# Performance work log

Hardware: AMD Instinct MI355X
Metric: run time of the kernel (lower is better)

The kernel has to match this reference:

```python
import jax, jax.numpy as jnp
import numpy as np

# Config matching init_kwargs: 63 single-grapheme tokens + optional blank -> C = 64,
# trivial (identity) lexicon, ngram = 0 (no transition model), allow_repeats = True.
# Under this config the GTN composition (target chain o lexicon -> tokens graph ->
# alignments, intersected with linear emission graph, forward_score) is exactly the
# CTC forward algorithm over the extended label sequence z = [blank, y1, blank, ...,
# yL, blank], with the s-2 -> s skip allowed for ALL non-blank states (allow_repeats).

B, T, C, L = 128, 3000, 64, 128
NEG = -1e30  # effective -inf, safe in fp32


def setup_inputs() -> dict:
    key = jax.random.key(0)
    k1, k2 = jax.random.split(key)
    inputs = jax.random.normal(k1, (B, T, C), dtype=jnp.float32)  # raw logits
    # target token ids in [0, C-2]; blank = C-1 is never a target
    targets = jax.random.randint(k2, (B, L), 0, C - 1, dtype=jnp.int32)
    return {"inputs": inputs, "targets": targets}


def reference(inputs, targets):
    Bv, Tv, Cv = inputs.shape
    Lv = targets.shape[1]
    S = 2 * Lv + 1
    blank = Cv - 1
    # transitions is None -> module applies log_softmax to inputs
    logp = jax.nn.log_softmax(inputs, axis=2)  # [B, T, C]
    # extended label sequence: blanks at even positions, targets at odd positions
    z = jnp.full((Bv, S), blank, dtype=jnp.int32).at[:, 1::2].set(targets)  # [B, S]
    # per-frame emission scores for each extended state: [B, T, S] -> [T, B, S]
    em = jnp.take_along_axis(logp, jnp.broadcast_to(z[:, None, :], (Bv, Tv, S)), axis=2)
    em = jnp.transpose(em, (1, 0, 2))
    # skip transition (s-2 -> s) allowed for every non-blank (odd) state because
    # allow_repeats=True (no z[s] != z[s-2] restriction)
    skip_ok = (jnp.arange(S) % 2 == 1)  # [S]

    alpha0 = (jnp.full((Bv, S), NEG, dtype=jnp.float32)
              .at[:, 0].set(em[0, :, 0])
              .at[:, 1].set(em[0, :, 1]))

    def step(alpha, e_t):
        a1 = jnp.pad(alpha[:, :-1], ((0, 0), (1, 0)), constant_values=NEG)
        a2 = jnp.pad(alpha[:, :-2], ((0, 0), (2, 0)), constant_values=NEG)
        a2 = jnp.where(skip_ok[None, :], a2, NEG)
        new = e_t + jax.scipy.special.logsumexp(jnp.stack([alpha, a1, a2], axis=0), axis=0)
        return new, None

    alphaT, _ = jax.lax.scan(step, alpha0, em[1:])  # [B, S]
    # accepting states: last label (S-2) and trailing blank (S-1)
    ll = jax.scipy.special.logsumexp(alphaT[:, S - 2:S], axis=1)  # [B]
    # reduction='none' -> scales = 1; forward returns torch.mean over batch
    return jnp.mean(-ll)
```

## Files before the change

kernel.cpp:

```cpp
#include <hip/hip_runtime.h>
#include <stdint.h>

#define BB 128
#define TT 3000
#define CC 64
#define LL 128
#define NEG (-1e30f)
#define LOG2E 1.4426950408889634f
#define LN2f 0.6931471805599453f
#define F 24
#define NCH 125
#define LSE_BLOCKS 512

typedef float f32x2 __attribute__((ext_vector_type(2)));

__device__ __forceinline__ float fexp2(float x) { return __builtin_amdgcn_exp2f(x); }
__device__ __forceinline__ float flog2(float x) { return __builtin_amdgcn_logf(x); }

__device__ __forceinline__ float lse2(float x, float y) {
    float m = fmaxf(x, y);
    float e = fexp2(-fabsf(x - y));
    return m + flog2(1.0f + e);
}
__device__ __forceinline__ float shr1_neg(float x) {
    int r = __builtin_amdgcn_update_dpp(__float_as_int(NEG), __float_as_int(x),
                                        0x138 , 0xF, 0xF, false);
    return __int_as_float(r);
}
#define SBAR() __builtin_amdgcn_sched_barrier(0)

__global__ __launch_bounds__(512) void fused_kernel(const float* __restrict__ in,
                                                    const int* __restrict__ tgt,
                                                    float* __restrict__ lse,
                                                    float* __restrict__ ll2) {
    __shared__ f32x2 ring[2][F][64];
    __shared__ float ringB[2][F];
    if (blockIdx.x < BB) {
        const int b = blockIdx.x;
        const int wave = threadIdx.x >> 6;
        const int lane = threadIdx.x & 63;
        const float* fb = in + (size_t)b * TT * CC;
        const int t0 = tgt[b * LL + 2 * lane];
        const int t1 = tgt[b * LL + 2 * lane + 1];

#define PRODUCE(cc, nb) {                                                        \
            const int tb_ = (cc) * F;                                            \
            const int p_ = wave - 1;                                             \
            float w1_[4], w3_[4], wb_[4];                                        \
            _Pragma("unroll")                                                    \
            for (int k = 0; k < 4; ++k) {                                        \
                int f_ = p_ + k * 7;                                             \
                if (f_ < F) {                                                    \
                    const float* fr_ = fb + (size_t)(tb_ + f_) * CC;             \
                    w1_[k] = fr_[t0]; w3_[k] = fr_[t1]; wb_[k] = fr_[63];        \
                }                                                                \
            }                                                                    \
            _Pragma("unroll")                                                    \
            for (int k = 0; k < 4; ++k) {                                        \
                int f_ = p_ + k * 7;                                             \
                if (f_ < F) {                                                    \
                    f32x2 v_; v_.x = w1_[k] * LOG2E; v_.y = w3_[k] * LOG2E;      \
                    ring[nb][f_][lane] = v_;                                     \
                    if (lane == 0) ringB[nb][f_] = wb_[k] * LOG2E;               \
                }                                                                \
            }                                                                    \
        }

        if (wave > 0) PRODUCE(0, 0);
        __syncthreads();

        if (wave == 0) {
            __builtin_amdgcn_s_setprio(1);
            const uint32_t ring_base =
                (uint32_t)(uintptr_t)&ring[0][0][0] + (uint32_t)lane * 8u;
            const uint32_t rb_base = (uint32_t)(uintptr_t)&ringB[0][0];

            float a0 = (lane == 0) ? 0.f : NEG;
            float a1 = NEG, a2 = NEG, a3 = NEG, a4 = NEG;

            for (int c = 0; c < NCH; ++c) {
                const uint32_t ra = ring_base + (uint32_t)(c & 1) * (F * 64 * 8);
                const uint32_t rb = rb_base + (uint32_t)(c & 1) * (F * 4);
                f32x2 e0, e1, e2; float b0, b1, b2;
                asm volatile("ds_read_b64 %0, %1 offset:0"   : "=v"(e0) : "v"(ra));
                asm volatile("ds_read_b32 %0, %1 offset:0"   : "=v"(b0) : "v"(rb));
                asm volatile("ds_read_b64 %0, %1 offset:512" : "=v"(e1) : "v"(ra));
                asm volatile("ds_read_b32 %0, %1 offset:4"   : "=v"(b1) : "v"(rb));
                #pragma unroll
                for (int j = 0; j < F; ++j) {
                    if (j + 2 < F) {
                        asm volatile("ds_read_b64 %0, %1 offset:%2"
                                     : "=v"(e2) : "v"(ra), "n"((j + 2) * 512));
                        asm volatile("ds_read_b32 %0, %1 offset:%2"
                                     : "=v"(b2) : "v"(rb), "n"((j + 2) * 4));
                        asm volatile("s_waitcnt lgkmcnt(4)" ::: "memory");
                    } else if (j + 2 == F) {
                        asm volatile("s_waitcnt lgkmcnt(2)" ::: "memory");
                    } else {
                        asm volatile("s_waitcnt lgkmcnt(0)" ::: "memory");
                    }
                    SBAR();
                    float pp = shr1_neg(a3);
                    float t_ = lse2(a0, pp);
                    float n0 = b0 + t_;
                    float n1 = e0.x + lse2(a1, t_);
                    float u_ = lse2(a2, a1);
                    float n2 = b0 + u_;
                    float n3 = e0.y + lse2(a3, u_);
                    float n4 = b0 + lse2(a4, a3);
                    a0 = n0; a1 = n1; a2 = n2; a3 = n3; a4 = n4;
                    e0 = e1; b0 = b1; e1 = e2; b1 = b2;
                }
                __syncthreads();
            }
            if (lane == 63) ll2[b] = lse2(a3, a4);
        } else {
            for (int c = 0; c < NCH; ++c) {
                if (c + 1 < NCH) PRODUCE(c + 1, (c + 1) & 1);
                __syncthreads();
            }
        }
        return;
    }
    int w = (blockIdx.x - BB) * 8 + (threadIdx.x >> 6);
    int lane = threadIdx.x & 63;
    const int stride = LSE_BLOCKS * 8;
    for (int row = w; row < BB * TT; row += stride) {
        float x = in[(size_t)row * CC + lane];
        float m = x;
        #pragma unroll
        for (int d = 32; d >= 1; d >>= 1) m = fmaxf(m, __shfl_xor(m, d, 64));
        float s = fexp2((x - m) * LOG2E);
        #pragma unroll
        for (int d = 32; d >= 1; d >>= 1) s += __shfl_xor(s, d, 64);
        if (lane == 0) lse[row] = m + flog2(s) * LN2f;
    }
}

__global__ __launch_bounds__(256) void bsum_kernel(const float* __restrict__ lse,
                                                   const float* __restrict__ ll2,
                                                   float* __restrict__ lossb) {
    __shared__ float red[256];
    int b = blockIdx.x;
    float s = 0.f;
    for (int i = threadIdx.x; i < TT; i += 256) s += lse[(size_t)b * TT + i];
    red[threadIdx.x] = s;
    __syncthreads();
    #pragma unroll
    for (int w = 128; w >= 1; w >>= 1) {
        if (threadIdx.x < w) red[threadIdx.x] += red[threadIdx.x + w];
        __syncthreads();
    }
    if (threadIdx.x == 0) lossb[b] = red[0] - ll2[b] * LN2f;
}

__global__ __launch_bounds__(64) void final_kernel(const float* __restrict__ lossb,
                                                   float* __restrict__ out) {
    int lane = threadIdx.x;
    float v = lossb[lane] + lossb[lane + 64];
    #pragma unroll
    for (int d = 32; d >= 1; d >>= 1) v += __shfl_xor(v, d, 64);
    if (lane == 0) out[0] = v / (float)BB;
}

extern "C" void kernel_launch(void* const* d_in, const int* in_sizes, int n_in,
                              void* d_out, int out_size, void* d_ws, size_t ws_size,
                              hipStream_t stream) {
    const float* in = (const float*)d_in[0];
    const int* tg = (const int*)d_in[1];
    float* out = (float*)d_out;
    float* lse = (float*)d_ws;
    float* ll2 = lse + (size_t)BB * TT;
    float* lossb = ll2 + BB;

    hipLaunchKernelGGL(fused_kernel, dim3(BB + LSE_BLOCKS), dim3(512), 0, stream,
                       in, tg, lse, ll2);
    hipLaunchKernelGGL(bsum_kernel, dim3(BB), dim3(256), 0, stream, lse, ll2, lossb);
    hipLaunchKernelGGL(final_kernel, dim3(1), dim3(64), 0, stream, lossb, out);
}
```

Before: 292.3 us.

## Split CTC alpha recursion across two waves with skewed pipelined boundary exchange

The serial CTC forward recursion, which previously ran five states per lane in one wave, is split across two waves that each hold two or three states per lane. The first wave covers the first half of the labels and writes its last lane's alpha into a shared boundary buffer each frame. The second wave runs one chunk behind and reads that boundary value. A three-slot emission ring makes room for the skew, and the producers drop to six waves. This shortens the per-frame dependency chain on the critical wave, at the cost of extra LDS traffic, a lag of one chunk, and an extra barrier phase.

New measurement: 241.2 us. 1.21x faster.

```diff
diff --git a/kernel.cpp b/kernel.cpp
--- a/kernel.cpp
+++ b/kernel.cpp
@@ -12,8 +12,6 @@
 #define NCH 125
 #define LSE_BLOCKS 512
 
-typedef float f32x2 __attribute__((ext_vector_type(2)));
-
 __device__ __forceinline__ float fexp2(float x) { return __builtin_amdgcn_exp2f(x); }
 __device__ __forceinline__ float flog2(float x) { return __builtin_amdgcn_logf(x); }
 
@@ -33,92 +31,153 @@
                                                     const int* __restrict__ tgt,
                                                     float* __restrict__ lse,
                                                     float* __restrict__ ll2) {
-    __shared__ f32x2 ring[2][F][64];
-    __shared__ float ringB[2][F];
+    __shared__ float ringT[3][F][128];
+    __shared__ float ringBl[3][F];
+    __shared__ float bndr[3][F];
+    __shared__ float dump[64];
     if (blockIdx.x < BB) {
         const int b = blockIdx.x;
         const int wave = threadIdx.x >> 6;
         const int lane = threadIdx.x & 63;
         const float* fb = in + (size_t)b * TT * CC;
-        const int t0 = tgt[b * LL + 2 * lane];
-        const int t1 = tgt[b * LL + 2 * lane + 1];
-
-#define PRODUCE(cc, nb) {                                                        \
-            const int tb_ = (cc) * F;                                            \
-            const int p_ = wave - 1;                                             \
-            float w1_[4], w3_[4], wb_[4];                                        \
-            _Pragma("unroll")                                                    \
-            for (int k = 0; k < 4; ++k) {                                        \
-                int f_ = p_ + k * 7;                                             \
-                if (f_ < F) {                                                    \
-                    const float* fr_ = fb + (size_t)(tb_ + f_) * CC;             \
-                    w1_[k] = fr_[t0]; w3_[k] = fr_[t1]; wb_[k] = fr_[63];        \
-                }                                                                \
-            }                                                                    \
-            _Pragma("unroll")                                                    \
-            for (int k = 0; k < 4; ++k) {                                        \
-                int f_ = p_ + k * 7;                                             \
-                if (f_ < F) {                                                    \
-                    f32x2 v_; v_.x = w1_[k] * LOG2E; v_.y = w3_[k] * LOG2E;      \
-                    ring[nb][f_][lane] = v_;                                     \
-                    if (lane == 0) ringB[nb][f_] = wb_[k] * LOG2E;               \
-                }                                                                \
-            }                                                                    \
-        }
-
-        if (wave > 0) PRODUCE(0, 0);
-        __syncthreads();
-
-        if (wave == 0) {
-            __builtin_amdgcn_s_setprio(1);
-            const uint32_t ring_base =
-                (uint32_t)(uintptr_t)&ring[0][0][0] + (uint32_t)lane * 8u;
-            const uint32_t rb_base = (uint32_t)(uintptr_t)&ringB[0][0];
-
-            float a0 = (lane == 0) ? 0.f : NEG;
-            float a1 = NEG, a2 = NEG, a3 = NEG, a4 = NEG;
-
-            for (int c = 0; c < NCH; ++c) {
-                const uint32_t ra = ring_base + (uint32_t)(c & 1) * (F * 64 * 8);
-                const uint32_t rb = rb_base + (uint32_t)(c & 1) * (F * 4);
-                f32x2 e0, e1, e2; float b0, b1, b2;
-                asm volatile("ds_read_b64 %0, %1 offset:0"   : "=v"(e0) : "v"(ra));
-                asm volatile("ds_read_b32 %0, %1 offset:0"   : "=v"(b0) : "v"(rb));
-                asm volatile("ds_read_b64 %0, %1 offset:512" : "=v"(e1) : "v"(ra));
-                asm volatile("ds_read_b32 %0, %1 offset:4"   : "=v"(b1) : "v"(rb));
+
+        if (wave >= 2) {
+            const int p = wave - 2;
+            const int t0 = tgt[b * LL + lane];
+            const int t1 = tgt[b * LL + 64 + lane];
+            auto produce = [&](int cc) {
+                const int slot = cc % 3;
+                const float* base = fb + (size_t)cc * F * CC;
+                float v0[4], v1[4], vb[4];
                 #pragma unroll
-                for (int j = 0; j < F; ++j) {
-                    if (j + 2 < F) {
-                        asm volatile("ds_read_b64 %0, %1 offset:%2"
-                                     : "=v"(e2) : "v"(ra), "n"((j + 2) * 512));
-                        asm volatile("ds_read_b32 %0, %1 offset:%2"
-                                     : "=v"(b2) : "v"(rb), "n"((j + 2) * 4));
-                        asm volatile("s_waitcnt lgkmcnt(4)" ::: "memory");
-                    } else if (j + 2 == F) {
-                        asm volatile("s_waitcnt lgkmcnt(2)" ::: "memory");
-                    } else {
-                        asm volatile("s_waitcnt lgkmcnt(0)" ::: "memory");
-                    }
-                    SBAR();
-                    float pp = shr1_neg(a3);
-                    float t_ = lse2(a0, pp);
-                    float n0 = b0 + t_;
-                    float n1 = e0.x + lse2(a1, t_);
-                    float u_ = lse2(a2, a1);
-                    float n2 = b0 + u_;
-                    float n3 = e0.y + lse2(a3, u_);
-                    float n4 = b0 + lse2(a4, a3);
-                    a0 = n0; a1 = n1; a2 = n2; a3 = n3; a4 = n4;
-                    e0 = e1; b0 = b1; e1 = e2; b1 = b2;
-                }
+                for (int k = 0; k < 4; ++k) {
+                    const float* fr = base + (p * 4 + k) * CC;
+                    v0[k] = fr[t0]; v1[k] = fr[t1]; vb[k] = fr[63];
+                }
+                #pragma unroll
+                for (int k = 0; k < 4; ++k) {
+                    int f = p * 4 + k;
+                    ringT[slot][f][lane] = v0[k] * LOG2E;
+                    ringT[slot][f][64 + lane] = v1[k] * LOG2E;
+                    if (lane == 0) ringBl[slot][f] = vb[k] * LOG2E;
+                }
+            };
+            produce(0);
+            __syncthreads();
+            for (int ph = 0; ph <= NCH; ++ph) {
+                if (ph + 1 < NCH) produce(ph + 1);
                 __syncthreads();
             }
-            if (lane == 63) ll2[b] = lse2(a3, a4);
-        } else {
-            for (int c = 0; c < NCH; ++c) {
-                if (c + 1 < NCH) PRODUCE(c + 1, (c + 1) & 1);
+        } else if (wave == 0) {
+            __builtin_amdgcn_s_setprio(1);
+            float a0 = (lane == 0) ? 0.f : NEG, a1 = NEG;
+            const uint32_t raT = (uint32_t)(uintptr_t)&ringT[0][0][0] + lane * 4u;
+            const uint32_t rbB = (uint32_t)(uintptr_t)&ringBl[0][0];
+            const uint32_t bnd0 = (uint32_t)(uintptr_t)&bndr[0][0];
+            const uint32_t dmp = (uint32_t)(uintptr_t)&dump[0] + lane * 4u;
+            const bool is63 = (lane == 63);
+            __syncthreads();
+            for (int ph = 0; ph <= NCH; ++ph) {
+                if (ph < NCH) {
+                    const int slot = ph % 3;
+                    const uint32_t ra = raT + slot * (F * 128 * 4);
+                    const uint32_t rb = rbB + slot * (F * 4);
+                    uint32_t wa = is63 ? (bnd0 + slot * (F * 4)) : dmp;
+                    const uint32_t wi = is63 ? 4u : 0u;
+                    float e0, e1, e2, b0, b1, b2;
+                    asm volatile("ds_read_b32 %0, %1 offset:0"   : "=v"(e0) : "v"(ra));
+                    asm volatile("ds_read_b32 %0, %1 offset:0"   : "=v"(b0) : "v"(rb));
+                    asm volatile("ds_read_b32 %0, %1 offset:512" : "=v"(e1) : "v"(ra));
+                    asm volatile("ds_read_b32 %0, %1 offset:4"   : "=v"(b1) : "v"(rb));
+                    #pragma unroll
+                    for (int j = 0; j < F; ++j) {
+                        if (j + 2 < F) {
+                            asm volatile("ds_read_b32 %0, %1 offset:%2"
+                                         : "=v"(e2) : "v"(ra), "n"((j + 2) * 512));
+                            asm volatile("ds_read_b32 %0, %1 offset:%2"
+                                         : "=v"(b2) : "v"(rb), "n"((j + 2) * 4));
+                            if (j == 0) asm volatile("s_waitcnt lgkmcnt(4)" ::: "memory");
+                            else        asm volatile("s_waitcnt lgkmcnt(5)" ::: "memory");
+                        } else if (j + 2 == F) {
+                            asm volatile("s_waitcnt lgkmcnt(3)" ::: "memory");
+                        } else {
+                            asm volatile("s_waitcnt lgkmcnt(1)" ::: "memory");
+                        }
+                        SBAR();
+                        float pm = shr1_neg(a1);
+                        float t_ = lse2(a0, pm);
+                        float n0 = b0 + t_;
+                        float n1 = e0 + lse2(a1, t_);
+                        a0 = n0; a1 = n1;
+                        asm volatile("ds_write_b32 %0, %1" :: "v"(wa), "v"(a1));
+                        wa += wi;
+                        e0 = e1; b0 = b1; e1 = e2; b1 = b2;
+                    }
+                }
                 __syncthreads();
             }
+        } else {
+            __builtin_amdgcn_s_setprio(1);
+            float a0 = NEG, a1 = NEG, a4 = NEG;
+            const uint32_t raT = (uint32_t)(uintptr_t)&ringT[0][0][0] + (64u + lane) * 4u;
+            const uint32_t rbB = (uint32_t)(uintptr_t)&ringBl[0][0];
+            const uint32_t bnd0 = (uint32_t)(uintptr_t)&bndr[0][0];
+            const bool is0 = (lane == 0);
+            __syncthreads();
+            for (int ph = 0; ph <= NCH; ++ph) {
+                if (ph >= 1) {
+                    const int c = ph - 1;
+                    const int slot = c % 3;
+                    const uint32_t ra = raT + slot * (F * 128 * 4);
+                    const uint32_t rb = rbB + slot * (F * 4);
+                    const uint32_t br = bnd0 + slot * (F * 4);
+                    float e0, e1, e2, b0, b1, b2, q0, q1, q2;
+                    if (c == 0) {
+                        q0 = NEG;
+                        asm volatile("ds_read_b32 %0, %1 offset:0"   : "=v"(e0) : "v"(ra));
+                        asm volatile("ds_read_b32 %0, %1 offset:0"   : "=v"(b0) : "v"(rb));
+                        asm volatile("ds_read_b32 %0, %1 offset:0"   : "=v"(q1) : "v"(br));
+                        asm volatile("ds_read_b32 %0, %1 offset:512" : "=v"(e1) : "v"(ra));
+                        asm volatile("ds_read_b32 %0, %1 offset:4"   : "=v"(b1) : "v"(rb));
+                    } else {
+                        const uint32_t pv = bnd0 + ((c - 1) % 3) * (F * 4);
+                        asm volatile("ds_read_b32 %0, %1 offset:%2"
+                                     : "=v"(q0) : "v"(pv), "n"((F - 1) * 4));
+                        asm volatile("ds_read_b32 %0, %1 offset:0"   : "=v"(e0) : "v"(ra));
+                        asm volatile("ds_read_b32 %0, %1 offset:0"   : "=v"(b0) : "v"(rb));
+                        asm volatile("ds_read_b32 %0, %1 offset:0"   : "=v"(q1) : "v"(br));
+                        asm volatile("ds_read_b32 %0, %1 offset:512" : "=v"(e1) : "v"(ra));
+                        asm volatile("ds_read_b32 %0, %1 offset:4"   : "=v"(b1) : "v"(rb));
+                    }
+                    #pragma unroll
+                    for (int j = 0; j < F; ++j) {
+                        if (j + 2 < F) {
+                            asm volatile("ds_read_b32 %0, %1 offset:%2"
+                                         : "=v"(e2) : "v"(ra), "n"((j + 2) * 512));
+                            asm volatile("ds_read_b32 %0, %1 offset:%2"
+                                         : "=v"(b2) : "v"(rb), "n"((j + 2) * 4));
+                            asm volatile("ds_read_b32 %0, %1 offset:%2"
+                                         : "=v"(q2) : "v"(br), "n"((j + 1) * 4));
+                            asm volatile("s_waitcnt lgkmcnt(6)" ::: "memory");
+                        } else if (j + 2 == F) {
+                            asm volatile("s_waitcnt lgkmcnt(3)" ::: "memory");
+                        } else {
+                            asm volatile("s_waitcnt lgkmcnt(0)" ::: "memory");
+                        }
+                        SBAR();
+                        float pm = shr1_neg(a1);
+                        pm = is0 ? q0 : pm;
+                        float t_ = lse2(a0, pm);
+                        float n0 = b0 + t_;
+                        float n1 = e0 + lse2(a1, t_);
+                        float n4 = b0 + lse2(a4, a1);
+                        a0 = n0; a1 = n1; a4 = n4;
+                        e0 = e1; b0 = b1; q0 = q1; e1 = e2; b1 = b2; q1 = q2;
+                    }
+                }
+                __syncthreads();
+            }
+            if (lane == 63) ll2[b] = lse2(a1, a4);
         }
         return;
     }
```
